# Optimization experiments

Measured on AMD Instinct MI355X. Metric: run time of the kernel, lower is better.

## Reference

```python
import jax, jax.numpy as jnp
import numpy as np

EPS = 1e-8
TEMP = 0.1

def setup_inputs() -> dict:
    key = jax.random.key(0)
    k1, k2, k3, k4, k5 = jax.random.split(key, 5)
    B, C, S, D = 4096, 1000, 5, 2048
    return {
        "query": jax.random.normal(k1, (B, D), dtype=jnp.float32),
        "labels": jax.random.randint(k2, (B,), 0, C),
        "memory_keys": jax.random.normal(k3, (C, S, D), dtype=jnp.float32),
        "memory_values": jax.random.normal(k4, (C, S, D), dtype=jnp.float32),
        "quality_scores": jax.random.uniform(k5, (C, S), dtype=jnp.float32),
        "top_k": 3,
    }

def reference(query, labels, memory_keys, memory_values, quality_scores, top_k):
    # Gather per-sample class slices: (B, S, D) and (B, S)
    class_keys = memory_keys[labels]
    class_vals = memory_values[labels]
    class_scores = quality_scores[labels]

    # Cosine similarity between query[i] and its class's slot keys
    qn = query / jnp.maximum(jnp.linalg.norm(query, axis=-1, keepdims=True), EPS)
    kn = class_keys / jnp.maximum(jnp.linalg.norm(class_keys, axis=-1, keepdims=True), EPS)
    sim = jnp.einsum('bd,bsd->bs', qn, kn)           # (B, S)
    combined = sim * class_scores                    # (B, S)

    k = min(int(top_k), class_scores.shape[1])
    top_scores, top_idx = jax.lax.top_k(combined, k) # (B, k)
    attn = jax.nn.softmax(top_scores / TEMP, axis=-1)
    top_vals = jnp.take_along_axis(class_vals, top_idx[..., None], axis=1)  # (B, k, D)
    retrieved = jnp.einsum('bk,bkd->bd', attn, top_vals)                    # (B, D)

    # miss handling: classes whose quality scores sum to 0 yield zeros
    hit = class_scores.sum(axis=1) != 0              # (B,)
    retrieved = jnp.where(hit[:, None], retrieved, 0.0)
    weights = jnp.where(hit, top_scores.mean(axis=-1), 0.0)
    return retrieved, weights
```

## Files before the change

kernel.cpp:

```cpp
#include <hip/hip_runtime.h>
#include <math.h>

#define NSLOT 5
#define EPSF 1e-8f

typedef float f4 __attribute__((ext_vector_type(4)));


__global__ void hist_kernel(const int* __restrict__ labels, int* __restrict__ counts, int B) {
    int i = blockIdx.x * blockDim.x + threadIdx.x;
    if (i < B) atomicAdd(&counts[labels[i]], 1);
}

__global__ void scan_kernel(const int* __restrict__ counts, int* __restrict__ cursor, int C) {
    __shared__ int sh[1024];
    __shared__ int running;
    if (threadIdx.x == 0) running = 0;
    __syncthreads();
    for (int base = 0; base < C; base += 1024) {
        int t = base + threadIdx.x;
        int v = (t < C) ? counts[t] : 0;
        sh[threadIdx.x] = v;
        __syncthreads();
        for (int d = 1; d < 1024; d <<= 1) {
            int x = (threadIdx.x >= d) ? sh[threadIdx.x - d] : 0;
            __syncthreads();
            sh[threadIdx.x] += x;
            __syncthreads();
        }
        int excl = sh[threadIdx.x] - v + running;
        if (t < C) cursor[t] = excl;
        __syncthreads();
        if (threadIdx.x == 0) running += sh[1023];
        __syncthreads();
    }
}

__global__ void scatter_kernel(const int* __restrict__ labels, int* __restrict__ cursor,
                               int* __restrict__ bucket, int B) {
    int i = blockIdx.x * blockDim.x + threadIdx.x;
    if (i < B) {
        int slot = atomicAdd(&cursor[labels[i]], 1);
        bucket[slot] = i;
    }
}


__global__ __launch_bounds__(256, 8) void mb_main_kernel(
    const float* __restrict__ query,
    const float* __restrict__ mkeys,
    const float* __restrict__ mvals,
    const float* __restrict__ qscores,
    const int*   __restrict__ topk_p,
    const int*   __restrict__ labels,
    const int*   __restrict__ bucket,
    float* __restrict__ out_ret,
    float* __restrict__ out_w,
    int B)
{
    const int tid  = threadIdx.x;
    const int lane = tid & 63;
    const int wave = tid >> 6;
    const int ws   = wave & 1;
    const int sidx = wave >> 1;

    int j;
    if (bucket) {
        j = (blockIdx.x & 7) * (B >> 3) + (blockIdx.x >> 3) * 2 + sidx;
    } else {
        j = blockIdx.x * 2 + sidx;
    }
    const bool active = (j < B);
    const int i = active ? (bucket ? bucket[j] : j) : 0;
    const int c = active ? labels[i] : 0;

    int k = topk_p[0];
    if (k > NSLOT) k = NSLOT;
    if (k < 1) k = 1;

    const int n4 = 512;
    const f4* q4 = reinterpret_cast<const f4*>(query) + (size_t)i * n4;
    const f4* k4 = reinterpret_cast<const f4*>(mkeys) + (size_t)c * NSLOT * n4;
    const f4* v4 = reinterpret_cast<const f4*>(mvals) + (size_t)c * NSLOT * n4;
    f4*       o4 = reinterpret_cast<f4*>(out_ret) + (size_t)i * n4;

    float qq = 0.f;
    float dot[NSLOT], kk[NSLOT];
#pragma unroll
    for (int s = 0; s < NSLOT; ++s) { dot[s] = 0.f; kk[s] = 0.f; }

    if (active) {
#pragma unroll
        for (int m = 0; m < 4; ++m) {
            const int idx = lane + (ws * 4 + m) * 64;
            f4 q = q4[idx];
            qq = fmaf(q.x, q.x, fmaf(q.y, q.y, fmaf(q.z, q.z, fmaf(q.w, q.w, qq))));
#pragma unroll
            for (int s = 0; s < NSLOT; ++s) {
                f4 kv = k4[s * n4 + idx];
                dot[s] = fmaf(q.x, kv.x, fmaf(q.y, kv.y, fmaf(q.z, kv.z, fmaf(q.w, kv.w, dot[s]))));
                kk[s]  = fmaf(kv.x, kv.x, fmaf(kv.y, kv.y, fmaf(kv.z, kv.z, fmaf(kv.w, kv.w, kk[s]))));
            }
        }
    }

#pragma unroll
    for (int off = 1; off < 64; off <<= 1) {
        qq += __shfl_xor(qq, off);
#pragma unroll
        for (int s = 0; s < NSLOT; ++s) {
            dot[s] += __shfl_xor(dot[s], off);
            kk[s]  += __shfl_xor(kk[s], off);
        }
    }

    __shared__ float red[2][2][11];
    if (lane == 0) {
        red[sidx][ws][0] = qq;
#pragma unroll
        for (int s = 0; s < NSLOT; ++s) {
            red[sidx][ws][1 + s] = dot[s];
            red[sidx][ws][6 + s] = kk[s];
        }
    }
    __syncthreads();
    qq = red[sidx][0][0] + red[sidx][1][0];
#pragma unroll
    for (int s = 0; s < NSLOT; ++s) {
        dot[s] = red[sidx][0][1 + s] + red[sidx][1][1 + s];
        kk[s]  = red[sidx][0][6 + s] + red[sidx][1][6 + s];
    }

    if (!active) return;

    float qn = fmaxf(sqrtf(qq), EPSF);

    float scr[NSLOT];
    float ssum = 0.f;
#pragma unroll
    for (int s = 0; s < NSLOT; ++s) {
        scr[s] = qscores[(size_t)c * NSLOT + s];
        ssum += scr[s];
    }

    float comb[NSLOT];
#pragma unroll
    for (int s = 0; s < NSLOT; ++s) {
        float kn = fmaxf(sqrtf(kk[s]), EPSF);
        comb[s] = (dot[s] / (qn * kn)) * scr[s];
    }

    bool used[NSLOT];
#pragma unroll
    for (int s = 0; s < NSLOT; ++s) used[s] = false;
    float tsc[NSLOT];
    int   tix[NSLOT];
#pragma unroll
    for (int jj = 0; jj < NSLOT; ++jj) {
        float best = -INFINITY;
        int bi = 0;
        if (jj < k) {
#pragma unroll
            for (int s = 0; s < NSLOT; ++s) {
                if (!used[s] && comb[s] > best) { best = comb[s]; bi = s; }
            }
#pragma unroll
            for (int s = 0; s < NSLOT; ++s) used[s] = used[s] || (s == bi);
        }
        tsc[jj] = best;
        tix[jj] = bi;
    }

    const bool hit = (ssum != 0.0f);
    float m = tsc[0];
    float esum = 0.f, wsum = 0.f;
    float a[NSLOT];
#pragma unroll
    for (int jj = 0; jj < NSLOT; ++jj) {
        if (jj < k) {
            a[jj] = __expf((tsc[jj] - m) * 10.0f);
            esum += a[jj];
            wsum += tsc[jj];
        } else {
            a[jj] = 0.f;
        }
    }
    float inv = hit ? (1.0f / esum) : 0.0f;

    if (ws == 0 && lane == 0) out_w[i] = hit ? (wsum / (float)k) : 0.0f;

    if (k == 3) {
        const float a0 = a[0] * inv, a1 = a[1] * inv, a2 = a[2] * inv;
        const f4* p0 = v4 + tix[0] * n4;
        const f4* p1 = v4 + tix[1] * n4;
        const f4* p2 = v4 + tix[2] * n4;
#pragma unroll
        for (int m2 = 0; m2 < 4; ++m2) {
            const int idx = lane + (ws * 4 + m2) * 64;
            f4 v0 = p0[idx];
            f4 v1 = p1[idx];
            f4 v2 = p2[idx];
            f4 acc;
            acc.x = fmaf(a0, v0.x, fmaf(a1, v1.x, a2 * v2.x));
            acc.y = fmaf(a0, v0.y, fmaf(a1, v1.y, a2 * v2.y));
            acc.z = fmaf(a0, v0.z, fmaf(a1, v1.z, a2 * v2.z));
            acc.w = fmaf(a0, v0.w, fmaf(a1, v1.w, a2 * v2.w));
            o4[idx] = acc;
        }
    } else {
        float wgt[NSLOT];
#pragma unroll
        for (int s = 0; s < NSLOT; ++s) {
            float wsv = 0.f;
#pragma unroll
            for (int jj = 0; jj < NSLOT; ++jj)
                if (jj < k && tix[jj] == s) wsv += a[jj] * inv;
            wgt[s] = wsv;
        }
#pragma unroll
        for (int m2 = 0; m2 < 4; ++m2) {
            const int idx = lane + (ws * 4 + m2) * 64;
            f4 acc = (f4)(0.f);
#pragma unroll
            for (int s = 0; s < NSLOT; ++s) {
                f4 v = v4[s * n4 + idx];
                acc.x = fmaf(wgt[s], v.x, acc.x);
                acc.y = fmaf(wgt[s], v.y, acc.y);
                acc.z = fmaf(wgt[s], v.z, acc.z);
                acc.w = fmaf(wgt[s], v.w, acc.w);
            }
            o4[idx] = acc;
        }
    }
}


__global__ __launch_bounds__(64) void mb_generic_kernel(
    const float* __restrict__ query,
    const int*   __restrict__ labels,
    const float* __restrict__ mkeys,
    const float* __restrict__ mvals,
    const float* __restrict__ qscores,
    const int*   __restrict__ topk_p,
    float* __restrict__ out_ret,
    float* __restrict__ out_w,
    int B, int n4)
{
    const int lane = threadIdx.x;
    const int i    = blockIdx.x;
    if (i >= B) return;
    const int c = labels[i];
    int k = topk_p[0];
    if (k > NSLOT) k = NSLOT;
    if (k < 1) k = 1;

    const f4* q4 = reinterpret_cast<const f4*>(query) + (size_t)i * n4;
    const f4* k4 = reinterpret_cast<const f4*>(mkeys) + (size_t)c * NSLOT * n4;
    const f4* v4 = reinterpret_cast<const f4*>(mvals) + (size_t)c * NSLOT * n4;
    f4*       o4 = reinterpret_cast<f4*>(out_ret) + (size_t)i * n4;

    float qq = 0.f, dot[NSLOT] = {0}, kk[NSLOT] = {0};
    for (int idx = lane; idx < n4; idx += 64) {
        f4 q = q4[idx];
        qq = fmaf(q.x, q.x, fmaf(q.y, q.y, fmaf(q.z, q.z, fmaf(q.w, q.w, qq))));
        for (int s = 0; s < NSLOT; ++s) {
            f4 t = k4[s * n4 + idx];
            dot[s] = fmaf(q.x, t.x, fmaf(q.y, t.y, fmaf(q.z, t.z, fmaf(q.w, t.w, dot[s]))));
            kk[s]  = fmaf(t.x, t.x, fmaf(t.y, t.y, fmaf(t.z, t.z, fmaf(t.w, t.w, kk[s]))));
        }
    }
    for (int o = 1; o < 64; o <<= 1) {
        qq += __shfl_xor(qq, o);
        for (int s = 0; s < NSLOT; ++s) {
            dot[s] += __shfl_xor(dot[s], o);
            kk[s]  += __shfl_xor(kk[s], o);
        }
    }
    float qn = fmaxf(sqrtf(qq), EPSF);
    float scr[NSLOT], ssum = 0.f;
    for (int s = 0; s < NSLOT; ++s) { scr[s] = qscores[(size_t)c * NSLOT + s]; ssum += scr[s]; }
    float comb[NSLOT];
    for (int s = 0; s < NSLOT; ++s)
        comb[s] = (dot[s] / (qn * fmaxf(sqrtf(kk[s]), EPSF))) * scr[s];
    bool used[NSLOT] = {false, false, false, false, false};
    float tsc[NSLOT]; int tix[NSLOT];
    for (int jj = 0; jj < NSLOT; ++jj) {
        float best = -INFINITY; int bi = 0;
        if (jj < k) {
            for (int s = 0; s < NSLOT; ++s)
                if (!used[s] && comb[s] > best) { best = comb[s]; bi = s; }
            used[bi] = true;
        }
        tsc[jj] = best; tix[jj] = bi;
    }
    const bool hit = (ssum != 0.0f);
    float m = tsc[0], esum = 0.f, wsum = 0.f, a[NSLOT];
    for (int jj = 0; jj < NSLOT; ++jj) {
        if (jj < k) { a[jj] = __expf((tsc[jj] - m) * 10.0f); esum += a[jj]; wsum += tsc[jj]; }
        else a[jj] = 0.f;
    }
    float inv = hit ? (1.0f / esum) : 0.0f;
    float w[NSLOT];
    for (int s = 0; s < NSLOT; ++s) {
        float wsv = 0.f;
        for (int jj = 0; jj < NSLOT; ++jj) if (jj < k && tix[jj] == s) wsv += a[jj] * inv;
        w[s] = wsv;
    }
    if (lane == 0) out_w[i] = hit ? (wsum / (float)k) : 0.0f;
    for (int idx = lane; idx < n4; idx += 64) {
        f4 acc = (f4)(0.f);
        for (int s = 0; s < NSLOT; ++s) {
            f4 v = v4[s * n4 + idx];
            acc += v * w[s];
        }
        o4[idx] = acc;
    }
}

extern "C" void kernel_launch(void* const* d_in, const int* in_sizes, int n_in,
                              void* d_out, int out_size, void* d_ws, size_t ws_size,
                              hipStream_t stream) {
    const float* query   = (const float*)d_in[0];
    const int*   labels  = (const int*)d_in[1];
    const float* mkeys   = (const float*)d_in[2];
    const float* mvals   = (const float*)d_in[3];
    const float* qscores = (const float*)d_in[4];
    const int*   topk    = (const int*)d_in[5];

    const int B  = in_sizes[1];
    const int D  = in_sizes[0] / B;
    const int n4 = D >> 2;
    const int C  = in_sizes[4] / NSLOT;

    float* out_ret = (float*)d_out;
    float* out_w   = out_ret + (size_t)B * D;

    if (D == 2048 && (B % 16 == 0) &&
        ((size_t)(2 * C + B) * sizeof(int) <= ws_size)) {
        int* counts = (int*)d_ws;
        int* cursor = counts + C;
        int* bkt    = counts + 2 * C;
        hipMemsetAsync(counts, 0, (size_t)C * sizeof(int), stream);
        hist_kernel<<<dim3((B + 255) / 256), dim3(256), 0, stream>>>(labels, counts, B);
        scan_kernel<<<dim3(1), dim3(1024), 0, stream>>>(counts, cursor, C);
        scatter_kernel<<<dim3((B + 255) / 256), dim3(256), 0, stream>>>(labels, cursor, bkt, B);

        mb_main_kernel<<<dim3(B / 2), dim3(256), 0, stream>>>(
            query, mkeys, mvals, qscores, topk, labels, bkt, out_ret, out_w, B);
    } else if (D == 2048) {
        mb_main_kernel<<<dim3((B + 1) / 2), dim3(256), 0, stream>>>(
            query, mkeys, mvals, qscores, topk, labels, nullptr, out_ret, out_w, B);
    } else {
        mb_generic_kernel<<<dim3(B), dim3(64), 0, stream>>>(
            query, labels, mkeys, mvals, qscores, topk, out_ret, out_w, B, n4);
    }
}
```

Before: 40.60 us.

## Assign one full wave per query row and drop cross-wave LDS reduction

Each query row is now handled by a single 64-lane wave covering all 2048 elements, where before two waves split the row. This removes the shared-memory reduction and the block-wide barrier, so every row is reduced with shuffles alone. Blocks grow to 512 threads holding 8 rows, and the bucketed path now requires B divisible by 64. Each wave does twice the serial work and keeps more loads in flight per thread, which may raise register pressure and lower parallelism per row.

New measurement: 42.55 us. 4.8% more time.

```diff
diff --git a/kernel.cpp b/kernel.cpp
--- a/kernel.cpp
+++ b/kernel.cpp
@@ -46,7 +46,7 @@
 }
 
 
-__global__ __launch_bounds__(256, 8) void mb_main_kernel(
+__global__ __launch_bounds__(512, 4) void mb_main_kernel(
     const float* __restrict__ query,
     const float* __restrict__ mkeys,
     const float* __restrict__ mvals,
@@ -61,18 +61,16 @@
     const int tid  = threadIdx.x;
     const int lane = tid & 63;
     const int wave = tid >> 6;
-    const int ws   = wave & 1;
-    const int sidx = wave >> 1;
 
     int j;
     if (bucket) {
-        j = (blockIdx.x & 7) * (B >> 3) + (blockIdx.x >> 3) * 2 + sidx;
+        j = (blockIdx.x & 7) * (B >> 3) + (blockIdx.x >> 3) * 8 + wave;
     } else {
-        j = blockIdx.x * 2 + sidx;
-    }
-    const bool active = (j < B);
-    const int i = active ? (bucket ? bucket[j] : j) : 0;
-    const int c = active ? labels[i] : 0;
+        j = blockIdx.x * 8 + wave;
+    }
+    if (j >= B) return;
+    const int i = bucket ? bucket[j] : j;
+    const int c = labels[i];
 
     int k = topk_p[0];
     if (k > NSLOT) k = NSLOT;
@@ -89,18 +87,16 @@
 #pragma unroll
     for (int s = 0; s < NSLOT; ++s) { dot[s] = 0.f; kk[s] = 0.f; }
 
-    if (active) {
-#pragma unroll
-        for (int m = 0; m < 4; ++m) {
-            const int idx = lane + (ws * 4 + m) * 64;
-            f4 q = q4[idx];
-            qq = fmaf(q.x, q.x, fmaf(q.y, q.y, fmaf(q.z, q.z, fmaf(q.w, q.w, qq))));
-#pragma unroll
-            for (int s = 0; s < NSLOT; ++s) {
-                f4 kv = k4[s * n4 + idx];
-                dot[s] = fmaf(q.x, kv.x, fmaf(q.y, kv.y, fmaf(q.z, kv.z, fmaf(q.w, kv.w, dot[s]))));
-                kk[s]  = fmaf(kv.x, kv.x, fmaf(kv.y, kv.y, fmaf(kv.z, kv.z, fmaf(kv.w, kv.w, kk[s]))));
-            }
+#pragma unroll
+    for (int m = 0; m < 8; ++m) {
+        const int idx = lane + m * 64;
+        f4 q = q4[idx];
+        qq = fmaf(q.x, q.x, fmaf(q.y, q.y, fmaf(q.z, q.z, fmaf(q.w, q.w, qq))));
+#pragma unroll
+        for (int s = 0; s < NSLOT; ++s) {
+            f4 kv = k4[s * n4 + idx];
+            dot[s] = fmaf(q.x, kv.x, fmaf(q.y, kv.y, fmaf(q.z, kv.z, fmaf(q.w, kv.w, dot[s]))));
+            kk[s]  = fmaf(kv.x, kv.x, fmaf(kv.y, kv.y, fmaf(kv.z, kv.z, fmaf(kv.w, kv.w, kk[s]))));
         }
     }
 
@@ -113,25 +109,6 @@
             kk[s]  += __shfl_xor(kk[s], off);
         }
     }
-
-    __shared__ float red[2][2][11];
-    if (lane == 0) {
-        red[sidx][ws][0] = qq;
-#pragma unroll
-        for (int s = 0; s < NSLOT; ++s) {
-            red[sidx][ws][1 + s] = dot[s];
-            red[sidx][ws][6 + s] = kk[s];
-        }
-    }
-    __syncthreads();
-    qq = red[sidx][0][0] + red[sidx][1][0];
-#pragma unroll
-    for (int s = 0; s < NSLOT; ++s) {
-        dot[s] = red[sidx][0][1 + s] + red[sidx][1][1 + s];
-        kk[s]  = red[sidx][0][6 + s] + red[sidx][1][6 + s];
-    }
-
-    if (!active) return;
 
     float qn = fmaxf(sqrtf(qq), EPSF);
 
@@ -172,13 +149,13 @@
     }
 
     const bool hit = (ssum != 0.0f);
-    float m = tsc[0];
+    float m0 = tsc[0];
     float esum = 0.f, wsum = 0.f;
     float a[NSLOT];
 #pragma unroll
     for (int jj = 0; jj < NSLOT; ++jj) {
         if (jj < k) {
-            a[jj] = __expf((tsc[jj] - m) * 10.0f);
+            a[jj] = __expf((tsc[jj] - m0) * 10.0f);
             esum += a[jj];
             wsum += tsc[jj];
         } else {
@@ -187,7 +164,7 @@
     }
     float inv = hit ? (1.0f / esum) : 0.0f;
 
-    if (ws == 0 && lane == 0) out_w[i] = hit ? (wsum / (float)k) : 0.0f;
+    if (lane == 0) out_w[i] = hit ? (wsum / (float)k) : 0.0f;
 
     if (k == 3) {
         const float a0 = a[0] * inv, a1 = a[1] * inv, a2 = a[2] * inv;
@@ -195,8 +172,8 @@
         const f4* p1 = v4 + tix[1] * n4;
         const f4* p2 = v4 + tix[2] * n4;
 #pragma unroll
-        for (int m2 = 0; m2 < 4; ++m2) {
-            const int idx = lane + (ws * 4 + m2) * 64;
+        for (int m = 0; m < 8; ++m) {
+            const int idx = lane + m * 64;
             f4 v0 = p0[idx];
             f4 v1 = p1[idx];
             f4 v2 = p2[idx];
@@ -218,8 +195,8 @@
             wgt[s] = wsv;
         }
 #pragma unroll
-        for (int m2 = 0; m2 < 4; ++m2) {
-            const int idx = lane + (ws * 4 + m2) * 64;
+        for (int m = 0; m < 8; ++m) {
+            const int idx = lane + m * 64;
             f4 acc = (f4)(0.f);
 #pragma unroll
             for (int s = 0; s < NSLOT; ++s) {
@@ -335,7 +312,7 @@
     float* out_ret = (float*)d_out;
     float* out_w   = out_ret + (size_t)B * D;
 
-    if (D == 2048 && (B % 16 == 0) &&
+    if (D == 2048 && (B % 64 == 0) &&
         ((size_t)(2 * C + B) * sizeof(int) <= ws_size)) {
         int* counts = (int*)d_ws;
         int* cursor = counts + C;
@@ -345,10 +322,10 @@
         scan_kernel<<<dim3(1), dim3(1024), 0, stream>>>(counts, cursor, C);
         scatter_kernel<<<dim3((B + 255) / 256), dim3(256), 0, stream>>>(labels, cursor, bkt, B);
 
-        mb_main_kernel<<<dim3(B / 2), dim3(256), 0, stream>>>(
+        mb_main_kernel<<<dim3(B / 8), dim3(512), 0, stream>>>(
             query, mkeys, mvals, qscores, topk, labels, bkt, out_ret, out_w, B);
     } else if (D == 2048) {
-        mb_main_kernel<<<dim3((B + 1) / 2), dim3(256), 0, stream>>>(
+        mb_main_kernel<<<dim3((B + 7) / 8), dim3(512), 0, stream>>>(
             query, mkeys, mvals, qscores, topk, labels, nullptr, out_ret, out_w, B);
     } else {
         mb_generic_kernel<<<dim3(B), dim3(64), 0, stream>>>(
```
